# Optimization experiments

Hardware: AMD Instinct MI355X
Metric: run time of the kernel (lower is better)

The kernel has to match this reference:

```python
import jax, jax.numpy as jnp
import numpy as np

N_NODES = 20000
IN_CH = 7
HID = 256
HEADS = 8
NEG_SLOPE = 0.2


def glorot(key, shape):
    fan = shape[0] + shape[-1] if len(shape) == 2 else int(np.prod(shape))
    lim = jnp.sqrt(6.0 / fan)
    return jax.random.uniform(key, shape, jnp.float32, -lim, lim)


def setup_inputs() -> dict:
    key = jax.random.key(0)
    ks = jax.random.split(key, 12)
    x = jax.random.normal(ks[0], (N_NODES, IN_CH), jnp.float32)
    edge_index = jax.random.randint(ks[1], (2, 160000), 0, N_NODES, jnp.int64)
    # conv1: in=7 -> heads=8, out=256, concat
    W1 = glorot(ks[2], (IN_CH, HEADS * HID))
    att_src1 = glorot(ks[3], (HEADS, HID))
    att_dst1 = glorot(ks[4], (HEADS, HID))
    b1 = jnp.zeros((HEADS * HID,), jnp.float32)
    # conv2: in=2048 -> heads=1, out=256, mean (concat=False)
    W2 = glorot(ks[5], (HEADS * HID, 1 * HID))
    att_src2 = glorot(ks[6], (1, HID))
    att_dst2 = glorot(ks[7], (1, HID))
    b2 = jnp.zeros((HID,), jnp.float32)
    return {"x": x, "edge_index": edge_index, "W1": W1, "att_src1": att_src1,
            "att_dst1": att_dst1, "b1": b1, "W2": W2, "att_src2": att_src2,
            "att_dst2": att_dst2, "b2": b2}


def gat_conv(x, src, dst, W, att_src, att_dst, bias, concat):
    # PyG GATConv (eval mode, dropout disabled)
    H, C = att_src.shape
    n = x.shape[0]
    h = (x @ W).reshape(n, H, C)                      # [N,H,C]
    a_src = jnp.sum(h * att_src[None], axis=-1)       # [N,H]
    a_dst = jnp.sum(h * att_dst[None], axis=-1)       # [N,H]
    alpha = a_src[src] + a_dst[dst]                   # [E,H]
    alpha = jax.nn.leaky_relu(alpha, NEG_SLOPE)
    # segment softmax over incoming edges of each destination node
    amax = jax.ops.segment_max(alpha, dst, num_segments=n)
    alpha = jnp.exp(alpha - amax[dst])
    denom = jax.ops.segment_sum(alpha, dst, num_segments=n)
    alpha = alpha / (denom[dst] + 1e-16)
    msg = h[src] * alpha[:, :, None]                  # [E,H,C] gather + weight
    out = jax.ops.segment_sum(msg, dst, num_segments=n)  # scatter-add aggregate
    out = out.reshape(n, H * C) if concat else out.mean(axis=1)
    return out + bias


def reference(x, edge_index, W1, att_src1, att_dst1, b1, W2, att_src2, att_dst2, b2):
    n = x.shape[0]
    # PyG GATConv default: add self-loops
    loops = jnp.arange(n, dtype=edge_index.dtype)
    src = jnp.concatenate([edge_index[0], loops])
    dst = jnp.concatenate([edge_index[1], loops])
    h = gat_conv(x, src, dst, W1, att_src1, att_dst1, b1, concat=True)
    h = jax.nn.elu(h)
    out = gat_conv(h, src, dst, W2, att_src2, att_dst2, b2, concat=False)
    return out
```

## Files before the change

### kernel.cpp

```cpp
#include <hip/hip_runtime.h>
#include <hip/hip_bf16.h>

#define N_NODES 20000
#define E_ORIG  160000
#define E_TOT   180000
#define HEADS   8
#define HID     256
#define F1      2048
#define NEG     0.2f
#define MAXDEG  96
#define GBKS    32
#define BMG     80

typedef __attribute__((ext_vector_type(8))) short  short8;
typedef __attribute__((ext_vector_type(4))) short  short4_;
typedef __attribute__((ext_vector_type(4))) float  f32x4;

__device__ inline float bf2f(ushort u){ union{unsigned u32; float f;} v; v.u32=((unsigned)u)<<16; return v.f; }
__device__ inline ushort f2bf(float f){
  union{float f; unsigned u;} v; v.f=f;
  unsigned lsb=(v.u>>16)&1u; v.u += 0x7fffu + lsb; return (ushort)(v.u>>16);
}

__device__ inline void gload16(const ushort* g, ushort* s){
  __builtin_amdgcn_global_load_lds((const __attribute__((address_space(1))) unsigned int*)g,
                                   (__attribute__((address_space(3))) unsigned int*)s, 16, 0, 0);
}

__global__ __launch_bounds__(256) void k_pre(const float* __restrict__ x, const float* __restrict__ W1,
    const float* __restrict__ as1, const float* __restrict__ ad1, const float* __restrict__ W2,
    float* __restrict__ a_src1, float* __restrict__ a_dst1, ushort* __restrict__ W2bT,
    int* __restrict__ cnt){
  __shared__ float s_w[128];
  __shared__ ushort sh[256][65];
  int tid = threadIdx.x, bid = blockIdx.x;
  if (tid < 128){
    int t = tid & 63;
    int k = t>>3, i = t&7;
    float v = 0.f;
    if (i < 7){
      const float* wp = W1 + i*F1 + (k<<8);
      const float* ap = ((tid<64) ? as1 : ad1) + (k<<8);
      f32x4 a4 = {0,0,0,0};
      for (int c=0;c<256;c+=4)
        a4 += (*(const f32x4*)&wp[c]) * (*(const f32x4*)&ap[c]);
      v = a4[0]+a4[1]+a4[2]+a4[3];
    }
    s_w[tid] = v;
  }
  __syncthreads();
  {
    int nl = tid>>3, k = tid&7;
    int n = bid*32 + nl;
    if (n < N_NODES){
      float s=0.f, d=0.f;
      const float* ws = &s_w[k*8];
      const float* wd = &s_w[64+k*8];
#pragma unroll
      for (int i=0;i<7;i++){
        float xv = x[n*7+i];
        s += xv*ws[i]; d += xv*wd[i];
      }
      a_src1[n*8+k]=s; a_dst1[n*8+k]=d;
    }
  }
  if (bid >= 32 && bid < 111){
    int i = (bid-32)*256 + tid;
    if (i < N_NODES) cnt[i] = 0;
  }
  if (bid < 32){
    int k0 = bid*64;
    for (int kk=0; kk<64; kk++) sh[tid][kk] = f2bf(W2[(size_t)(k0+kk)*256 + tid]);
    __syncthreads();
#pragma unroll
    for (int c8=0; c8<8; c8++){
      short8 v;
#pragma unroll
      for (int j=0;j<8;j++) v[j] = (short)sh[tid][c8*8+j];
      *(short8*)&W2bT[(size_t)tid*F1 + k0 + c8*8] = v;
    }
  }
}

__global__ void k_scat(const int* __restrict__ ei, int* __restrict__ cnt, int* __restrict__ bucket){
  int e = blockIdx.x*256 + threadIdx.x;
  if (e >= E_TOT) return;
  int s, d;
  if (e < E_ORIG){ s = ei[e]; d = ei[E_ORIG + e]; }
  else           { s = d = e - E_ORIG; }
  int pos = atomicAdd(&cnt[d], 1);
  if (pos < MAXDEG) bucket[d*MAXDEG + pos] = s;
}

__global__ __launch_bounds__(512) void k_sa1(const int* __restrict__ cnt, const int* __restrict__ bucket,
    const float* __restrict__ a_src1, const float* __restrict__ a_dst1,
    const float* __restrict__ x, const float* __restrict__ W1, const float* __restrict__ b1,
    ushort* __restrict__ x2){
  __shared__ float sxa[8][64];
  int tid = threadIdx.x, wv = tid>>6, lane = tid&63;
  int n = blockIdx.x*8 + wv;
  {
    int k = lane>>3, i = lane&7;
    int ie = (i==7)?0:i;
    int base = n*MAXDEG;
    int deg  = cnt[n]; if (deg>MAXDEG) deg=MAXDEG;
    float ad = a_dst1[n*8+k];
    int src0 = (lane<deg)    ? bucket[base+lane]    : 0;
    int src1 = (lane+64<deg) ? bucket[base+lane+64] : 0;
    float denom = 0.f, acc = 0.f;
    int j = 0;
    for (; j+2<=deg; j+=2){
      int s0 = (j<64)   ? __shfl(src0,j)     : __shfl(src1,j-64);
      int s1 = (j+1<64) ? __shfl(src0,j+1)   : __shfl(src1,j-63);
      float A0 = a_src1[(size_t)s0*8+k] + ad;
      float A1 = a_src1[(size_t)s1*8+k] + ad;
      float X0 = x[(size_t)s0*7+ie];
      float X1 = x[(size_t)s1*7+ie];
      A0 = (A0>0.f)?A0:NEG*A0;  A1 = (A1>0.f)?A1:NEG*A1;
      float w0 = __expf(A0),   w1 = __expf(A1);
      denom += w0; acc += w0*X0;
      denom += w1; acc += w1*X1;
    }
    if (j<deg){
      int s0 = (j<64) ? __shfl(src0,j) : __shfl(src1,j-64);
      float A0 = a_src1[(size_t)s0*8+k] + ad;
      A0 = (A0>0.f)?A0:NEG*A0;
      float w0 = __expf(A0);
      denom += w0; acc += w0*x[(size_t)s0*7+ie];
    }
    sxa[wv][lane] = acc/denom;
  }
  __syncthreads();
  int kh = tid>>6, c4 = (tid&63)<<2;
  f32x4 w1r[7];
#pragma unroll
  for (int i=0;i<7;i++) w1r[i] = *(const f32x4*)(W1 + i*F1 + (kh<<8) + c4);
  f32x4 bb = *(const f32x4*)(b1 + (kh<<8) + c4);
#pragma unroll
  for (int g=0; g<8; g++){
    int nn = blockIdx.x*8 + g;
    const float* xa = &sxa[g][kh<<3];
    f32x4 h = bb;
#pragma unroll
    for (int i=0;i<7;i++) h += xa[i]*w1r[i];
    short4_ o;
#pragma unroll
    for (int j=0;j<4;j++){ float v=h[j]; v=(v>0.f)?v:(__expf(v)-1.f); o[j]=(short)f2bf(v); }
    *(short4_*)(x2 + (size_t)nn*F1 + (kh<<8) + c4) = o;
  }
}

__global__ __launch_bounds__(256) void k_gemm2m(const ushort* __restrict__ A,
    const ushort* __restrict__ BT, ushort* __restrict__ h2b,
    const float* __restrict__ as2, const float* __restrict__ ad2,
    float* __restrict__ a_src2, float* __restrict__ a_dst2){
  __shared__ __align__(16) ushort S[2][(BMG+256)*64];
  int tid = threadIdx.x;
  int m0 = blockIdx.x*BMG;
  int w = tid>>6, l = tid&63;
  int lrow = l&15, lk = l>>4;
  int nc = w<<6;

  const ushort* gp[11];
#pragma unroll
  for (int rep=0;rep<11;rep++){
    int lin = rep*256 + tid;
    if (lin < BMG*8){
      int r = lin>>3, s = lin&7;
      gp[rep] = A + (size_t)(m0+r)*F1 + ((s ^ (r&7))<<3);
    } else if (lin < (BMG+256)*8){
      int j = lin - BMG*8;
      int c = j>>3, s = j&7;
      gp[rep] = BT + (size_t)c*F1 + ((s ^ (c&7))<<3);
    } else gp[rep] = BT;
  }

  f32x4 acc[5][4] = {};

#pragma unroll
  for (int rep=0;rep<10;rep++) gload16(gp[rep], &S[0][(rep*256+tid)<<3]);
  if (tid < 128) gload16(gp[10], &S[0][(10*256+tid)<<3]);
  __syncthreads();

  int cur = 0;
  for (int t=0; t<GBKS; t++){
    if (t+1 < GBKS){
      int k0 = (t+1)<<6;
#pragma unroll
      for (int rep=0;rep<10;rep++) gload16(gp[rep]+k0, &S[cur^1][(rep*256+tid)<<3]);
      if (tid < 128) gload16(gp[10]+k0, &S[cur^1][(10*256+tid)<<3]);
    }
    const ushort* as_ = &S[cur][0];
    const ushort* bs_ = &S[cur][BMG*64];
#pragma unroll
    for (int kk=0;kk<2;kk++){
      short8 af[5], bfr[4];
#pragma unroll
      for (int m=0;m<5;m++){
        int r = (m<<4) + lrow;
        af[m] = *(const short8*)&as_[(r<<6) + ((((kk<<2)|lk) ^ (r&7))<<3)];
      }
#pragma unroll
      for (int n=0;n<4;n++){
        int c = nc + (n<<4) + lrow;
        bfr[n] = *(const short8*)&bs_[(c<<6) + ((((kk<<2)|lk) ^ (c&7))<<3)];
      }
#pragma unroll
      for (int m=0;m<5;m++)
#pragma unroll
        for (int n=0;n<4;n++)
          acc[m][n] = __builtin_amdgcn_mfma_f32_16x16x32_bf16(af[m], bfr[n], acc[m][n], 0,0,0);
    }
    __syncthreads();
    cur ^= 1;
  }

  float* sps = (float*)&S[0][0];
  float* spd = sps + BMG*4;
  float s2v[4], d2v[4];
#pragma unroll
  for (int n=0;n<4;n++){
    int col = nc + (n<<4) + lrow;
    s2v[n]=as2[col]; d2v[n]=ad2[col];
  }
#pragma unroll
  for (int m=0;m<5;m++){
#pragma unroll
    for (int j=0;j<4;j++){
      int lr = (m<<4) + (lk<<2) + j;
      int grow = m0 + lr;
      float ps=0.f, pd=0.f;
#pragma unroll
      for (int n=0;n<4;n++){
        float v = acc[m][n][j];
        ps += v*s2v[n]; pd += v*d2v[n];
        h2b[(size_t)grow*256 + nc+(n<<4)+lrow] = f2bf(v);
      }
      ps += __shfl_xor(ps,8); ps += __shfl_xor(ps,4); ps += __shfl_xor(ps,2); ps += __shfl_xor(ps,1);
      pd += __shfl_xor(pd,8); pd += __shfl_xor(pd,4); pd += __shfl_xor(pd,2); pd += __shfl_xor(pd,1);
      if (lrow==0){
        sps[(lr<<2) | w] = ps;
        spd[(lr<<2) | w] = pd;
      }
    }
  }
  __syncthreads();
  if (tid < BMG){
    int grow = m0 + tid;
    f32x4 a = *(const f32x4*)&sps[tid<<2];
    f32x4 b = *(const f32x4*)&spd[tid<<2];
    a_src2[grow] = a[0]+a[1]+a[2]+a[3];
    a_dst2[grow] = b[0]+b[1]+b[2]+b[3];
  }
}

__global__ __launch_bounds__(512) void k_agg2(const int* __restrict__ cnt, const int* __restrict__ bucket,
    const float* __restrict__ a_src2, const float* __restrict__ a_dst2, const ushort* __restrict__ h2b,
    const float* __restrict__ b2, float* __restrict__ out){
  int tid = threadIdx.x, wv = tid>>6, lane = tid&63;
  int n = blockIdx.x*8 + wv;
  int base = n*MAXDEG;
  int deg  = cnt[n]; if (deg > MAXDEG) deg = MAXDEG;
  float ad = a_dst2[n];

  int src0 = (lane<deg)     ? bucket[base+lane]    : 0;
  int src1 = (lane+64<deg)  ? bucket[base+lane+64] : 0;
  float e0 = 0.f, e1 = 0.f;
  if (lane<deg)   { float a = a_src2[src0]+ad; a = (a>0.f)?a:NEG*a; e0 = __expf(a); }
  if (lane+64<deg){ float a = a_src2[src1]+ad; a = (a>0.f)?a:NEG*a; e1 = __expf(a); }
  float s = e0+e1;
  for (int off=32; off; off>>=1) s += __shfl_xor(s,off);
  float inv = 1.f/(s+1e-16f);
  e0 *= inv; e1 *= inv;

  int c0 = lane<<2;
  float acc0=0.f, acc1=0.f, acc2=0.f, acc3=0.f;
  int d1 = (deg<64)?deg:64;
  for (int j=0;j<d1;j++){
    float w = __shfl(e0, j);
    int  sj = __shfl(src0, j);
    short4_ hv = *(const short4_*)(h2b + (size_t)sj*256 + c0);
    acc0 += w*bf2f((ushort)hv[0]); acc1 += w*bf2f((ushort)hv[1]);
    acc2 += w*bf2f((ushort)hv[2]); acc3 += w*bf2f((ushort)hv[3]);
  }
  for (int j=64;j<deg;j++){
    float w = __shfl(e1, j-64);
    int  sj = __shfl(src1, j-64);
    short4_ hv = *(const short4_*)(h2b + (size_t)sj*256 + c0);
    acc0 += w*bf2f((ushort)hv[0]); acc1 += w*bf2f((ushort)hv[1]);
    acc2 += w*bf2f((ushort)hv[2]); acc3 += w*bf2f((ushort)hv[3]);
  }
  f32x4 bb = *(const f32x4*)(b2 + c0);
  f32x4 o; o[0]=acc0+bb[0]; o[1]=acc1+bb[1]; o[2]=acc2+bb[2]; o[3]=acc3+bb[3];
  *(f32x4*)(out + (size_t)n*256 + c0) = o;
}

extern "C" void kernel_launch(void* const* d_in, const int* in_sizes, int n_in,
                              void* d_out, int out_size, void* d_ws, size_t ws_size,
                              hipStream_t stream){
  const float* x      = (const float*)d_in[0];
  const int*   ei     = (const int*)  d_in[1];
  const float* W1     = (const float*)d_in[2];
  const float* att_s1 = (const float*)d_in[3];
  const float* att_d1 = (const float*)d_in[4];
  const float* b1     = (const float*)d_in[5];
  const float* W2     = (const float*)d_in[6];
  const float* att_s2 = (const float*)d_in[7];
  const float* att_d2 = (const float*)d_in[8];
  const float* b2     = (const float*)d_in[9];
  float* out = (float*)d_out;

  char* p = (char*)d_ws;
  auto alloc = [&](size_t bytes)->char*{ char* r = p; p += (bytes + 255) & ~(size_t)255; return r; };
  ushort* x2    = (ushort*)alloc((size_t)N_NODES*F1*2);
  ushort* W2bT  = (ushort*)alloc((size_t)F1*256*2);
  ushort* h2b   = (ushort*)alloc((size_t)N_NODES*256*2);
  float*  a_src1= (float*) alloc((size_t)N_NODES*8*4);
  float*  a_dst1= (float*) alloc((size_t)N_NODES*8*4);
  float*  a_src2= (float*) alloc((size_t)N_NODES*4);
  float*  a_dst2= (float*) alloc((size_t)N_NODES*4);
  int*    cnt   = (int*)   alloc((size_t)N_NODES*4);
  int*    bucket= (int*)   alloc((size_t)N_NODES*MAXDEG*4);

  k_pre    <<<(N_NODES+31)/32, 256, 0, stream>>>(x, W1, att_s1, att_d1, W2,
                                                 a_src1, a_dst1, W2bT, cnt);
  k_scat   <<<(E_TOT+255)/256, 256, 0, stream>>>(ei, cnt, bucket);
  k_sa1    <<<N_NODES/8, 512, 0, stream>>>(cnt, bucket, a_src1, a_dst1, x, W1, b1, x2);
  k_gemm2m <<<N_NODES/BMG, 256, 0, stream>>>(x2, W2bT, h2b, att_s2, att_d2, a_src2, a_dst2);
  k_agg2   <<<N_NODES/8, 512, 0, stream>>>(cnt, bucket, a_src2, a_dst2, h2b, b2, out);
}
```

Baseline: 119.4 us.

## Fold layer-2 attention vectors into W2 and compute scores in sa1

```diff
diff --git a/kernel.cpp b/kernel.cpp
--- a/kernel.cpp
+++ b/kernel.cpp
@@ -29,8 +29,9 @@
 
 __global__ __launch_bounds__(256) void k_pre(const float* __restrict__ x, const float* __restrict__ W1,
     const float* __restrict__ as1, const float* __restrict__ ad1, const float* __restrict__ W2,
+    const float* __restrict__ as2, const float* __restrict__ ad2,
     float* __restrict__ a_src1, float* __restrict__ a_dst1, ushort* __restrict__ W2bT,
-    int* __restrict__ cnt){
+    float* __restrict__ ws2, float* __restrict__ wd2, int* __restrict__ cnt){
   __shared__ float s_w[128];
   __shared__ ushort sh[256][65];
   int tid = threadIdx.x, bid = blockIdx.x;
@@ -68,6 +69,20 @@
     int i = (bid-32)*256 + tid;
     if (i < N_NODES) cnt[i] = 0;
   }
+  if (bid >= 111 && bid < 367){
+    int r = (bid-111)*8 + (tid>>5);
+    int l32 = tid&31;
+    float ps=0.f, pd=0.f;
+#pragma unroll
+    for (int it=0; it<8; it++){
+      int j = l32 + it*32;
+      float w = W2[(size_t)r*256 + j];
+      ps += w*as2[j]; pd += w*ad2[j];
+    }
+#pragma unroll
+    for (int off=16; off; off>>=1){ ps += __shfl_xor(ps,off); pd += __shfl_xor(pd,off); }
+    if (l32==0){ ws2[r]=ps; wd2[r]=pd; }
+  }
   if (bid < 32){
     int k0 = bid*64;
     for (int kk=0; kk<64; kk++) sh[tid][kk] = f2bf(W2[(size_t)(k0+kk)*256 + tid]);
@@ -95,8 +110,10 @@
 __global__ __launch_bounds__(512) void k_sa1(const int* __restrict__ cnt, const int* __restrict__ bucket,
     const float* __restrict__ a_src1, const float* __restrict__ a_dst1,
     const float* __restrict__ x, const float* __restrict__ W1, const float* __restrict__ b1,
-    ushort* __restrict__ x2){
+    const float* __restrict__ ws2, const float* __restrict__ wd2,
+    ushort* __restrict__ x2, float* __restrict__ a_src2, float* __restrict__ a_dst2){
   __shared__ float sxa[8][64];
+  __shared__ float sred[8][8][2];
   int tid = threadIdx.x, wv = tid>>6, lane = tid&63;
   int n = blockIdx.x*8 + wv;
   {
@@ -135,7 +152,9 @@
   f32x4 w1r[7];
 #pragma unroll
   for (int i=0;i<7;i++) w1r[i] = *(const f32x4*)(W1 + i*F1 + (kh<<8) + c4);
-  f32x4 bb = *(const f32x4*)(b1 + (kh<<8) + c4);
+  f32x4 bb   = *(const f32x4*)(b1  + (kh<<8) + c4);
+  f32x4 ws2v = *(const f32x4*)(ws2 + (kh<<8) + c4);
+  f32x4 wd2v = *(const f32x4*)(wd2 + (kh<<8) + c4);
 #pragma unroll
   for (int g=0; g<8; g++){
     int nn = blockIdx.x*8 + g;
@@ -144,16 +163,31 @@
 #pragma unroll
     for (int i=0;i<7;i++) h += xa[i]*w1r[i];
     short4_ o;
-#pragma unroll
-    for (int j=0;j<4;j++){ float v=h[j]; v=(v>0.f)?v:(__expf(v)-1.f); o[j]=(short)f2bf(v); }
+    float ps = 0.f, pd = 0.f;
+#pragma unroll
+    for (int j=0;j<4;j++){
+      float v=h[j]; v=(v>0.f)?v:(__expf(v)-1.f);
+      o[j]=(short)f2bf(v);
+      ps += v*ws2v[j]; pd += v*wd2v[j];
+    }
     *(short4_*)(x2 + (size_t)nn*F1 + (kh<<8) + c4) = o;
+#pragma unroll
+    for (int off=32; off; off>>=1){ ps += __shfl_xor(ps,off); pd += __shfl_xor(pd,off); }
+    if (lane==0){ sred[g][wv][0]=ps; sred[g][wv][1]=pd; }
+  }
+  __syncthreads();
+  if (tid < 16){
+    int g = tid>>1, sel = tid&1;
+    float s = 0.f;
+#pragma unroll
+    for (int w8=0; w8<8; w8++) s += sred[g][w8][sel];
+    int nn = blockIdx.x*8 + g;
+    if (sel) a_dst2[nn] = s; else a_src2[nn] = s;
   }
 }
 
 __global__ __launch_bounds__(256) void k_gemm2m(const ushort* __restrict__ A,
-    const ushort* __restrict__ BT, ushort* __restrict__ h2b,
-    const float* __restrict__ as2, const float* __restrict__ ad2,
-    float* __restrict__ a_src2, float* __restrict__ a_dst2){
+    const ushort* __restrict__ BT, ushort* __restrict__ h2b){
   __shared__ __align__(16) ushort S[2][(BMG+256)*64];
   int tid = threadIdx.x;
   int m0 = blockIdx.x*BMG;
@@ -215,42 +249,15 @@
     cur ^= 1;
   }
 
-  float* sps = (float*)&S[0][0];
-  float* spd = sps + BMG*4;
-  float s2v[4], d2v[4];
-#pragma unroll
-  for (int n=0;n<4;n++){
-    int col = nc + (n<<4) + lrow;
-    s2v[n]=as2[col]; d2v[n]=ad2[col];
-  }
 #pragma unroll
   for (int m=0;m<5;m++){
 #pragma unroll
     for (int j=0;j<4;j++){
-      int lr = (m<<4) + (lk<<2) + j;
-      int grow = m0 + lr;
-      float ps=0.f, pd=0.f;
-#pragma unroll
-      for (int n=0;n<4;n++){
-        float v = acc[m][n][j];
-        ps += v*s2v[n]; pd += v*d2v[n];
-        h2b[(size_t)grow*256 + nc+(n<<4)+lrow] = f2bf(v);
-      }
-      ps += __shfl_xor(ps,8); ps += __shfl_xor(ps,4); ps += __shfl_xor(ps,2); ps += __shfl_xor(ps,1);
-      pd += __shfl_xor(pd,8); pd += __shfl_xor(pd,4); pd += __shfl_xor(pd,2); pd += __shfl_xor(pd,1);
-      if (lrow==0){
-        sps[(lr<<2) | w] = ps;
-        spd[(lr<<2) | w] = pd;
-      }
-    }
-  }
-  __syncthreads();
-  if (tid < BMG){
-    int grow = m0 + tid;
-    f32x4 a = *(const f32x4*)&sps[tid<<2];
-    f32x4 b = *(const f32x4*)&spd[tid<<2];
-    a_src2[grow] = a[0]+a[1]+a[2]+a[3];
-    a_dst2[grow] = b[0]+b[1]+b[2]+b[3];
+      int grow = m0 + (m<<4) + (lk<<2) + j;
+#pragma unroll
+      for (int n=0;n<4;n++)
+        h2b[(size_t)grow*256 + nc+(n<<4)+lrow] = f2bf(acc[m][n][j]);
+    }
   }
 }
 
@@ -319,13 +326,16 @@
   float*  a_dst1= (float*) alloc((size_t)N_NODES*8*4);
   float*  a_src2= (float*) alloc((size_t)N_NODES*4);
   float*  a_dst2= (float*) alloc((size_t)N_NODES*4);
+  float*  ws2   = (float*) alloc((size_t)F1*4);
+  float*  wd2   = (float*) alloc((size_t)F1*4);
   int*    cnt   = (int*)   alloc((size_t)N_NODES*4);
   int*    bucket= (int*)   alloc((size_t)N_NODES*MAXDEG*4);
 
-  k_pre    <<<(N_NODES+31)/32, 256, 0, stream>>>(x, W1, att_s1, att_d1, W2,
-                                                 a_src1, a_dst1, W2bT, cnt);
+  k_pre    <<<(N_NODES+31)/32, 256, 0, stream>>>(x, W1, att_s1, att_d1, W2, att_s2, att_d2,
+                                                 a_src1, a_dst1, W2bT, ws2, wd2, cnt);
   k_scat   <<<(E_TOT+255)/256, 256, 0, stream>>>(ei, cnt, bucket);
-  k_sa1    <<<N_NODES/8, 512, 0, stream>>>(cnt, bucket, a_src1, a_dst1, x, W1, b1, x2);
-  k_gemm2m <<<N_NODES/BMG, 256, 0, stream>>>(x2, W2bT, h2b, att_s2, att_d2, a_src2, a_dst2);
+  k_sa1    <<<N_NODES/8, 512, 0, stream>>>(cnt, bucket, a_src1, a_dst1, x, W1, b1,
+                                           ws2, wd2, x2, a_src2, a_dst2);
+  k_gemm2m <<<N_NODES/BMG, 256, 0, stream>>>(x2, W2bT, h2b);
   k_agg2   <<<N_NODES/8, 512, 0, stream>>>(cnt, bucket, a_src2, a_dst2, h2b, b2, out);
 }
```

Result: slower. 126.3 us (+5.7%).
